# Optimization experiments

Measured on AMD Instinct MI355X. Metric: run time of the kernel, lower is better.

The kernel has to match this reference:

```python
import jax, jax.numpy as jnp
import numpy as np

B, T, H = 4, 2048, 1024
BUD = 512
S = max(8, BUD)
S += S % 2
HALF = S // 2
LOC = max(H, 2 * BUD)


def setup_inputs() -> dict:
    key = jax.random.key(0)
    ks = jax.random.split(key, 16)
    def w(k, i, o):
        return jax.random.normal(k, (i, o), jnp.float32) / np.sqrt(i).astype(np.float32)
    return {
        "x": jax.random.normal(ks[0], (B, T, H), jnp.float32),
        "W_rf": w(ks[1], H, S), "W_ri": w(ks[2], H, S), "W_rv": w(ks[3], H, S),
        "W_rq": w(ks[4], H, S), "W_ro": w(ks[5], S, H),
        "W_sw": w(ks[6], H, S), "W_sg": w(ks[7], H, S), "W_som": w(ks[8], H, HALF),
        "W_sd": w(ks[9], H, S), "W_sq": w(ks[10], H, S), "W_so": w(ks[11], S, H),
        "W_up": w(ks[12], H, LOC), "W_gate": w(ks[13], H, LOC), "W_down": w(ks[14], LOC, H),
        "W_mix": w(ks[15], H, 3),
        "read_init": jnp.zeros((S,), jnp.float32),
        "stable_init": jnp.zeros((S,), jnp.float32),
    }


def reference(x, W_rf, W_ri, W_rv, W_rq, W_ro, W_sw, W_sg, W_som, W_sd, W_sq, W_so,
              W_up, W_gate, W_down, W_mix, read_init, stable_init):
    silu = jax.nn.silu
    # Precompute all per-token projections as batched GEMMs: [B,T,*]
    rf = jnp.tanh(x @ W_rf)                      # read forget
    rg = jax.nn.sigmoid(x @ W_ri)                # read input gate
    rc = silu(x @ W_rv)                          # read candidate
    omega = jnp.pi * jnp.tanh(x @ W_som)         # [B,T,HALF]
    cosw, sinw = jnp.cos(omega), jnp.sin(omega)
    damp = jnp.exp(-jax.nn.softplus(x @ W_sd))
    sg = jax.nn.sigmoid(x @ W_sg)
    sc = silu(x @ W_sw)

    def step(carry, inputs):
        rs, ss = carry
        rf_t, rg_t, rc_t, cw, sw_, dp, sg_t, sc_t = inputs
        rs = rf_t * rs + rg_t * rc_t
        even, odd = ss[:, :HALF], ss[:, HALF:]
        rot = jnp.concatenate([cw * even - sw_ * odd, sw_ * even + cw * odd], axis=-1)
        ss = dp * rot + sg_t * sc_t
        return (rs, ss), (rs, ss)

    init = (jnp.broadcast_to(read_init, (B, S)), jnp.broadcast_to(stable_init, (B, S)))
    seq = tuple(jnp.swapaxes(a, 0, 1) for a in (rf, rg, rc, cosw, sinw, damp, sg, sc))
    _, (rs_seq, ss_seq) = jax.lax.scan(step, init, seq)
    rs_seq = jnp.swapaxes(rs_seq, 0, 1)  # [B,T,S]
    ss_seq = jnp.swapaxes(ss_seq, 0, 1)

    read_f = silu((x @ W_rq) * rs_seq) @ W_ro
    stable_f = silu((x @ W_sq) * ss_seq) @ W_so
    local_f = ((x @ W_up) * silu(x @ W_gate)) @ W_down
    mw = jax.nn.softmax(x @ W_mix, axis=-1)  # [B,T,3]
    out = mw[..., 0:1] * read_f + mw[..., 1:2] * stable_f + mw[..., 2:3] * local_f
    return out
```

## Files before the change

kernel.cpp:

```cpp
#include <hip/hip_runtime.h>

#define B_    4
#define T_    2048
#define H_    1024
#define S_    512
#define HALF_ 256
#define LOC_  1024
#define BT_   8192
#define N1_   6400
#define K1_   1024
#define N2_   1024
#define K2_   2048
#define NCH_  32
#define LC_   64

typedef __attribute__((ext_vector_type(8))) short  bf16x8;
typedef __attribute__((ext_vector_type(4))) float  f32x4;
typedef __attribute__((ext_vector_type(4))) unsigned short u16x4;

__device__ __forceinline__ float b2f(unsigned short u) {
    union { unsigned i; float f; } v; v.i = ((unsigned)u) << 16; return v.f;
}
__device__ __forceinline__ unsigned short f2b(float f) {
    union { float f; unsigned i; } v; v.f = f;
    unsigned r = v.i + 0x7fffu + ((v.i >> 16) & 1u);
    return (unsigned short)(r >> 16);
}
__device__ __forceinline__ float rcp_(float x) { return __builtin_amdgcn_rcpf(x); }
__device__ __forceinline__ float sigm_(float v) { return rcp_(1.f + __expf(-v)); }
__device__ __forceinline__ float silu_(float v) { return v * rcp_(1.f + __expf(-v)); }
__device__ __forceinline__ float tanh_(float v) { return 1.f - 2.f * rcp_(1.f + __expf(2.f * v)); }

__device__ __forceinline__ void gload16(const void* g, void* l) {
    __builtin_amdgcn_global_load_lds(
        (const __attribute__((address_space(1))) void*)g,
        (__attribute__((address_space(3))) void*)l,
        16, 0, 0);
}

__global__ void prep_x(const float* __restrict__ x, const float* __restrict__ Wm,
                       unsigned short* __restrict__ xb, float4* __restrict__ mw) {
    const int row  = blockIdx.x * 4 + (threadIdx.x >> 6);
    const int lane = threadIdx.x & 63;
    const float4* xr = (const float4*)(x + (size_t)row * H_);
    u16x4* xbr = (u16x4*)(xb + (size_t)row * H_);
    float s0 = 0.f, s1 = 0.f, s2 = 0.f;
#pragma unroll
    for (int p = 0; p < 4; p++) {
        const int k4 = p * 64 + lane;
        float4 v = xr[k4];
        u16x4 u;
        u.x = f2b(v.x); u.y = f2b(v.y); u.z = f2b(v.z); u.w = f2b(v.w);
        xbr[k4] = u;
        const int k3 = k4 * 12;
        s0 += v.x * Wm[k3 + 0] + v.y * Wm[k3 + 3] + v.z * Wm[k3 + 6] + v.w * Wm[k3 + 9];
        s1 += v.x * Wm[k3 + 1] + v.y * Wm[k3 + 4] + v.z * Wm[k3 + 7] + v.w * Wm[k3 + 10];
        s2 += v.x * Wm[k3 + 2] + v.y * Wm[k3 + 5] + v.z * Wm[k3 + 8] + v.w * Wm[k3 + 11];
    }
#pragma unroll
    for (int off = 32; off; off >>= 1) {
        s0 += __shfl_down(s0, off);
        s1 += __shfl_down(s1, off);
        s2 += __shfl_down(s2, off);
    }
    if (lane == 0) {
        float m = fmaxf(s0, fmaxf(s1, s2));
        float e0 = __expf(s0 - m), e1 = __expf(s1 - m), e2 = __expf(s2 - m);
        float inv = 1.f / (e0 + e1 + e2);
        mw[row] = (float4){ e0 * inv, e1 * inv, e2 * inv, 0.f };
    }
}

struct TOp { const float* src; int Kw; int Nw; int n_ofs; int k_ofs; int which; };
struct TOps { TOp v[14]; };

__global__ void pack_w_kernel(TOps ops, unsigned short* __restrict__ w1, unsigned short* __restrict__ w2) {
    TOp op = ops.v[blockIdx.z];
    int kt = blockIdx.x * 32, nt = blockIdx.y * 32;
    if (kt >= op.Kw || nt >= op.Nw) return;
    __shared__ float tile[32][33];
    int tx = threadIdx.x & 31, ty = threadIdx.x >> 5;
#pragma unroll
    for (int r = 0; r < 4; r++) {
        int k = kt + ty + r * 8;
        tile[ty + r * 8][tx] = op.src[(size_t)k * op.Nw + nt + tx];
    }
    __syncthreads();
    unsigned short* dst = op.which ? w2 : w1;
    int stride = op.which ? K2_ : K1_;
#pragma unroll
    for (int r = 0; r < 4; r++) {
        int n = nt + ty + r * 8;
        dst[(size_t)(op.n_ofs + n) * stride + op.k_ofs + kt + tx] = f2b(tile[tx][ty + r * 8]);
    }
}

#define STAGE(kt_, dA, dB) {          \
    gload16(aP0 + (kt_), (dA));       \
    gload16(aP1 + (kt_), (dA) + 512); \
    gload16(bP0 + (kt_), (dB));       \
    gload16(bP1 + (kt_), (dB) + 512); }

#define COMPUTE(sAr, sBr) {                                                            \
    bf16x8 af[4], bfv[4];                                                              \
    _Pragma("unroll")                                                                  \
    for (int m_ = 0; m_ < 4; m_++)                                                     \
        af[m_] = *(const bf16x8*)((sAr) + (wm + m_ * 16 + fr) * 32 + rsl);             \
    _Pragma("unroll")                                                                  \
    for (int n_ = 0; n_ < 4; n_++)                                                     \
        bfv[n_] = *(const bf16x8*)((sBr) + (wn + n_ * 16 + fr) * 32 + rsl);            \
    _Pragma("unroll")                                                                  \
    for (int m_ = 0; m_ < 4; m_++)                                                     \
        _Pragma("unroll")                                                              \
        for (int n_ = 0; n_ < 4; n_++)                                                 \
            acc[m_][n_] = __builtin_amdgcn_mfma_f32_16x16x32_bf16(af[m_], bfv[n_], acc[m_][n_], 0, 0, 0); }

template<int MODE>
__global__ __launch_bounds__(256, 3) void gemm_bf16(
    const unsigned short* __restrict__ A,
    const unsigned short* __restrict__ Bt,
    void* __restrict__ Cout,
    unsigned short* __restrict__ swb,
    const int M, const int N, const int K)
{
    __shared__ __align__(16) char smem[32768];
    unsigned short* sA0 = (unsigned short*)smem;
    unsigned short* sB0 = (unsigned short*)(smem + 8192);
    unsigned short* sA1 = (unsigned short*)(smem + 16384);
    unsigned short* sB1 = (unsigned short*)(smem + 24576);
    const int tid  = threadIdx.x;
    const int wid  = tid >> 6;
    const int lane = tid & 63;

    const int flat = blockIdx.y * gridDim.x + blockIdx.x;
    const int xcd  = flat & 7;
    const int ii   = flat >> 3;
    const int bm   = ((xcd << 3) + (ii & 7)) * 128;
    const int bn   = (ii >> 3) * 128;

    const int wm = (wid >> 1) * 64;
    const int wn = (wid & 1) * 64;

    f32x4 acc[4][4];
#pragma unroll
    for (int m = 0; m < 4; m++)
#pragma unroll
        for (int n = 0; n < 4; n++) acc[m][n] = (f32x4){0.f, 0.f, 0.f, 0.f};

    const int r0 = wid * 32 + (lane >> 2);
    const int sl = ((lane & 3) ^ ((r0 >> 1) & 3)) * 8;
    const unsigned short* aP0 = A  + (size_t)(bm + r0)      * K + sl;
    const unsigned short* aP1 = A  + (size_t)(bm + r0 + 16) * K + sl;
    const unsigned short* bP0 = Bt + (size_t)(bn + r0)      * K + sl;
    const unsigned short* bP1 = Bt + (size_t)(bn + r0 + 16) * K + sl;
    unsigned short* wA0 = sA0 + wid * 1024;
    unsigned short* wB0 = sB0 + wid * 1024;
    unsigned short* wA1 = sA1 + wid * 1024;
    unsigned short* wB1 = sB1 + wid * 1024;

    const int fr  = lane & 15;
    const int h   = lane >> 4;
    const int rsl = (h ^ ((fr >> 1) & 3)) * 8;
    const int nt  = K >> 5;

    STAGE(0, wA0, wB0);
    __syncthreads();
    for (int t = 0; t < nt; t += 2) {
        STAGE((t + 1) * 32, wA1, wB1);
        COMPUTE(sA0, sB0);
        __syncthreads();
        if (t + 2 < nt) STAGE((t + 2) * 32, wA0, wB0);
        COMPUTE(sA1, sB1);
        __syncthreads();
    }

    if (MODE == 0) {
        float* outp = (float*)Cout;
        float* wp = (float*)(smem + wid * 4608);
#pragma unroll
        for (int m = 0; m < 4; m++) {
#pragma unroll
            for (int n = 0; n < 4; n++)
#pragma unroll
                for (int r = 0; r < 4; r++)
                    wp[(h * 4 + r) * 68 + n * 16 + fr] = acc[m][n][r];
#pragma unroll
            for (int rnd = 0; rnd < 4; rnd++) {
                int lr = rnd * 4 + (lane >> 4);
                int lc = (lane & 15) * 4;
                float4 v = *(float4*)&wp[lr * 68 + lc];
                int grow = bm + wm + m * 16 + lr;
                int gcol = bn + wn + lc;
                *(float4*)&outp[(size_t)grow * N + gcol] = v;
            }
        }
    } else {
        int reg;
        if      (bn < 512)  reg = 0;
        else if (bn < 1024) reg = 1;
        else if (bn < 1536) reg = 2;
        else if (bn < 2048) reg = 3;
        else if (bn < 2560) reg = 2;
        else if (bn < 3072) reg = 1;
        else if (bn < 3584) reg = 4;
        else if (bn < 4096) reg = 3;
        else if (bn < 4352) reg = 5;
        else if (bn < 5376) reg = 3;
        else                reg = 2;

        unsigned short* proj = (unsigned short*)Cout;
        unsigned short* wp = (unsigned short*)(smem + wid * 2304);
        const int nsub = (reg == 5) ? 2 : 1;
#pragma unroll
        for (int m = 0; m < 4; m++) {
            for (int sub = 0; sub < nsub; sub++) {
#pragma unroll
                for (int n = 0; n < 4; n++)
#pragma unroll
                    for (int r = 0; r < 4; r++) {
                        float v = acc[m][n][r];
                        float o;
                        if      (reg == 0) o = tanh_(v);
                        else if (reg == 1) o = sigm_(v);
                        else if (reg == 2) o = silu_(v);
                        else if (reg == 3) o = v;
                        else if (reg == 4) o = sigm_(-v);
                        else {
                            float om = 3.14159265358979f * tanh_(v);
                            o = sub ? __sinf(om) : __cosf(om);
                        }
                        wp[(h * 4 + r) * 72 + n * 16 + fr] = f2b(o);
                    }
#pragma unroll
                for (int p = 0; p < 2; p++) {
                    int lr = p * 8 + (lane >> 3);
                    int lc = (lane & 7) * 8;
                    bf16x8 v = *(bf16x8*)(wp + lr * 72 + lc);
                    int grow = bm + wm + m * 16 + lr;
                    int gcol = bn + wn + lc;
                    if (sub == 0)
                        *(bf16x8*)(proj + (size_t)grow * N + gcol) = v;
                    else
                        *(bf16x8*)(swb + (size_t)grow * HALF_ + (gcol - 4096)) = v;
                }
            }
        }
    }
}

__global__ void scan_pass1(const unsigned short* __restrict__ proj, const unsigned short* __restrict__ swb,
                           float* __restrict__ rsP, float* __restrict__ rsY,
                           float4* __restrict__ ssM, float2* __restrict__ ssY) {
    const int c = blockIdx.x, b = blockIdx.y, z = blockIdx.z, tid = threadIdx.x;
    const int row0 = b * T_ + c * LC_;
    const unsigned short* base = proj + (size_t)row0 * N1_;
    if (z < 2) {
        const int s = z * 256 + tid;
        float P = 1.f, y = 0.f;
#pragma unroll 4
        for (int t = 0; t < LC_; t++) {
            const unsigned short* r = base + (size_t)t * N1_;
            float rf = b2f(r[s]);
            float rg = b2f(r[512 + s]);
            float rc = b2f(r[1024 + s]);
            y = rf * y + rg * rc;
            P *= rf;
        }
        int idx = (b * NCH_ + c) * S_ + s;
        rsP[idx] = P; rsY[idx] = y;
    } else {
        const int p = tid;
        const unsigned short* swr = swb + (size_t)row0 * HALF_;
        float m00 = 1.f, m01 = 0.f, m10 = 0.f, m11 = 1.f, y0 = 0.f, y1 = 0.f;
#pragma unroll 2
        for (int t = 0; t < LC_; t++) {
            const unsigned short* r = base + (size_t)t * N1_;
            float cw  = b2f(r[4096 + p]);
            float sw  = b2f(swr[(size_t)t * HALF_ + p]);
            float de  = b2f(r[3072 + p]);
            float dob = b2f(r[3328 + p]);
            float ge  = b2f(r[2560 + p]);
            float go  = b2f(r[2816 + p]);
            float ce  = b2f(r[2048 + p]);
            float co  = b2f(r[2304 + p]);
            float a = de * cw, bb = -de * sw, cc = dob * sw, dd = dob * cw;
            float ny0 = a * y0 + bb * y1 + ge * ce;
            float ny1 = cc * y0 + dd * y1 + go * co;
            y0 = ny0; y1 = ny1;
            float n00 = a * m00 + bb * m10, n01 = a * m01 + bb * m11;
            float n10 = cc * m00 + dd * m10, n11 = cc * m01 + dd * m11;
            m00 = n00; m01 = n01; m10 = n10; m11 = n11;
        }
        int idx = (b * NCH_ + c) * HALF_ + p;
        ssM[idx] = (float4){m00, m01, m10, m11};
        ssY[idx] = (float2){y0, y1};
    }
}

__global__ void scan_pass2(const float* __restrict__ rsP, const float* __restrict__ rsY,
                           const float4* __restrict__ ssM, const float2* __restrict__ ssY,
                           const float* __restrict__ read_init, const float* __restrict__ stable_init,
                           float* __restrict__ rsStart, float2* __restrict__ ssStart) {
    int id = blockIdx.x * 256 + threadIdx.x;
    if (id < B_ * S_) {
        int b = id / S_, s = id % S_;
        float st = read_init[s];
        for (int c = 0; c < NCH_; c++) {
            int idx = (b * NCH_ + c) * S_ + s;
            rsStart[idx] = st;
            st = rsP[idx] * st + rsY[idx];
        }
    } else {
        id -= B_ * S_;
        int b = id / HALF_, p = id % HALF_;
        float y0 = stable_init[p], y1 = stable_init[p + HALF_];
        for (int c = 0; c < NCH_; c++) {
            int idx = (b * NCH_ + c) * HALF_ + p;
            ssStart[idx] = (float2){y0, y1};
            float4 m = ssM[idx]; float2 u = ssY[idx];
            float ny0 = m.x * y0 + m.y * y1 + u.x;
            float ny1 = m.z * y0 + m.w * y1 + u.y;
            y0 = ny0; y1 = ny1;
        }
    }
}

__global__ void scan_pass3(const unsigned short* __restrict__ proj, const unsigned short* __restrict__ swb,
                           const float* __restrict__ rsStart, const float2* __restrict__ ssStart,
                           const float4* __restrict__ mw, unsigned short* __restrict__ G) {
    const int c = blockIdx.x, b = blockIdx.y, z = blockIdx.z, tid = threadIdx.x;
    const int row0 = b * T_ + c * LC_;
    const unsigned short* base = proj + (size_t)row0 * N1_;
    if (z < 2) {
        const int s = z * 256 + tid;
        float rs = rsStart[(b * NCH_ + c) * S_ + s];
#pragma unroll 4
        for (int t = 0; t < LC_; t++) {
            const size_t row = row0 + t;
            const unsigned short* r = base + (size_t)t * N1_;
            float rf = b2f(r[s]);
            float rg = b2f(r[512 + s]);
            float rc = b2f(r[1024 + s]);
            rs = rf * rs + rg * rc;
            float q  = b2f(r[1536 + s]);
            float zz = q * rs;
            G[row * 2048 + s] = f2b(mw[row].x * silu_(zz));
        }
    } else {
        const int p = tid;
        const unsigned short* swr = swb + (size_t)row0 * HALF_;
        float2 st = ssStart[(b * NCH_ + c) * HALF_ + p];
        float y0 = st.x, y1 = st.y;
#pragma unroll 2
        for (int t = 0; t < LC_; t++) {
            const size_t row = row0 + t;
            const unsigned short* r = base + (size_t)t * N1_;
            float cw  = b2f(r[4096 + p]);
            float sw  = b2f(swr[(size_t)t * HALF_ + p]);
            float de  = b2f(r[3072 + p]);
            float dob = b2f(r[3328 + p]);
            float ge  = b2f(r[2560 + p]);
            float go  = b2f(r[2816 + p]);
            float ce  = b2f(r[2048 + p]);
            float co  = b2f(r[2304 + p]);
            float a = de * cw, bb = -de * sw, cc = dob * sw, dd = dob * cw;
            float ny0 = a * y0 + bb * y1 + ge * ce;
            float ny1 = cc * y0 + dd * y1 + go * co;
            y0 = ny0; y1 = ny1;
            float qe = b2f(r[3584 + p]);
            float qo = b2f(r[3840 + p]);
            float w1v = mw[row].y;
            G[row * 2048 + 512 + p] = f2b(w1v * silu_(qe * y0));
            G[row * 2048 + 768 + p] = f2b(w1v * silu_(qo * y1));
        }
    }
}

__global__ void local_ew(const unsigned short* __restrict__ proj, const float4* __restrict__ mw,
                         unsigned short* __restrict__ G) {
    int i   = blockIdx.x * 256 + threadIdx.x;
    int row = i >> 7;
    int j   = (i & 127) * 8;
    bf16x8 up = *(const bf16x8*)(proj + (size_t)row * N1_ + 4352 + j);
    bf16x8 gs = *(const bf16x8*)(proj + (size_t)row * N1_ + 5376 + j);
    float m2 = mw[row].z;
    bf16x8 o;
#pragma unroll
    for (int e = 0; e < 8; e++)
        o[e] = (short)f2b(m2 * b2f((unsigned short)up[e]) * b2f((unsigned short)gs[e]));
    *(bf16x8*)(G + (size_t)row * 2048 + 1024 + j) = o;
}

extern "C" void kernel_launch(void* const* d_in, const int* in_sizes, int n_in,
                              void* d_out, int out_size, void* d_ws, size_t ws_size,
                              hipStream_t stream) {
    const float* x       = (const float*)d_in[0];
    const float* W_rf    = (const float*)d_in[1];
    const float* W_ri    = (const float*)d_in[2];
    const float* W_rv    = (const float*)d_in[3];
    const float* W_rq    = (const float*)d_in[4];
    const float* W_ro    = (const float*)d_in[5];
    const float* W_sw    = (const float*)d_in[6];
    const float* W_sg    = (const float*)d_in[7];
    const float* W_som   = (const float*)d_in[8];
    const float* W_sd    = (const float*)d_in[9];
    const float* W_sq    = (const float*)d_in[10];
    const float* W_so    = (const float*)d_in[11];
    const float* W_up    = (const float*)d_in[12];
    const float* W_gate  = (const float*)d_in[13];
    const float* W_down  = (const float*)d_in[14];
    const float* W_mix   = (const float*)d_in[15];
    const float* read_init   = (const float*)d_in[16];
    const float* stable_init = (const float*)d_in[17];

    char* ws = (char*)d_ws;
    size_t off = 0;
    auto alloc = [&](size_t bytes) -> void* {
        void* p = ws + off;
        off = (off + bytes + 255) & ~(size_t)255;
        return p;
    };
    unsigned short* xb   = (unsigned short*)alloc((size_t)BT_ * H_ * 2);
    unsigned short* w1   = (unsigned short*)alloc((size_t)N1_ * K1_ * 2);
    unsigned short* w2   = (unsigned short*)alloc((size_t)N2_ * K2_ * 2);
    unsigned short* proj = (unsigned short*)alloc((size_t)BT_ * N1_ * 2);
    unsigned short* swb  = (unsigned short*)alloc((size_t)BT_ * HALF_ * 2);
    float4*         mw   = (float4*)alloc((size_t)BT_ * 16);
    unsigned short* G    = (unsigned short*)alloc((size_t)BT_ * 2048 * 2);
    float*  rsP     = (float*) alloc((size_t)B_ * NCH_ * S_ * 4);
    float*  rsY     = (float*) alloc((size_t)B_ * NCH_ * S_ * 4);
    float4* ssM     = (float4*)alloc((size_t)B_ * NCH_ * HALF_ * 16);
    float2* ssY     = (float2*)alloc((size_t)B_ * NCH_ * HALF_ * 8);
    float*  rsStart = (float*) alloc((size_t)B_ * NCH_ * S_ * 4);
    float2* ssStart = (float2*)alloc((size_t)B_ * NCH_ * HALF_ * 8);
    if (off > ws_size) return;

    prep_x<<<BT_ / 4, 256, 0, stream>>>(x, W_mix, xb, mw);

    TOps ops;
    int i = 0;
    auto add = [&](const float* s, int Kw, int Nw, int n_ofs, int k_ofs, int which) {
        ops.v[i].src = s; ops.v[i].Kw = Kw; ops.v[i].Nw = Nw;
        ops.v[i].n_ofs = n_ofs; ops.v[i].k_ofs = k_ofs; ops.v[i].which = which; i++;
    };
    add(W_rf,  1024,  512,    0,    0, 0);
    add(W_ri,  1024,  512,  512,    0, 0);
    add(W_rv,  1024,  512, 1024,    0, 0);
    add(W_rq,  1024,  512, 1536,    0, 0);
    add(W_sw,  1024,  512, 2048,    0, 0);
    add(W_sg,  1024,  512, 2560,    0, 0);
    add(W_sd,  1024,  512, 3072,    0, 0);
    add(W_sq,  1024,  512, 3584,    0, 0);
    add(W_som, 1024,  256, 4096,    0, 0);
    add(W_up,  1024, 1024, 4352,    0, 0);
    add(W_gate,1024, 1024, 5376,    0, 0);
    add(W_ro,   512, 1024,    0,    0, 1);
    add(W_so,   512, 1024,    0,  512, 1);
    add(W_down,1024, 1024,    0, 1024, 1);
    pack_w_kernel<<<dim3(32, 32, 14), 256, 0, stream>>>(ops, w1, w2);

    gemm_bf16<1><<<dim3(N1_ / 128, BT_ / 128), 256, 0, stream>>>(xb, w1, (void*)proj, swb, BT_, N1_, K1_);

    scan_pass1<<<dim3(NCH_, B_, 3), 256, 0, stream>>>(proj, swb, rsP, rsY, ssM, ssY);
    scan_pass2<<<12, 256, 0, stream>>>(rsP, rsY, ssM, ssY, read_init, stable_init, rsStart, ssStart);
    scan_pass3<<<dim3(NCH_, B_, 3), 256, 0, stream>>>(proj, swb, rsStart, ssStart, mw, G);

    local_ew<<<(BT_ * LOC_ / 8) / 256, 256, 0, stream>>>(proj, mw, G);

    gemm_bf16<0><<<dim3(N2_ / 128, BT_ / 128), 256, 0, stream>>>(G, w2, d_out, nullptr, BT_, N2_, K2_);
}
```

Baseline: 273.7 us.

## Fuse local gated-MLP elementwise into projection GEMM epilogue via interleaved up/gate weights

Packs the W_up and W_gate columns interleaved in 16-column groups so each warp's accumulator holds matching up and gate values. The first GEMM's epilogue then computes mix-weight * up * silu(gate) directly and writes bf16 into G, and the separate local_ew kernel is removed. This avoids writing up/gate projections to proj and reading them back in another kernel. In exchange the epilogue gains per-row mw loads and a new store pattern.

```diff
diff --git a/kernel.cpp b/kernel.cpp
--- a/kernel.cpp
+++ b/kernel.cpp
@@ -71,7 +71,7 @@
     }
 }
 
-struct TOp { const float* src; int Kw; int Nw; int n_ofs; int k_ofs; int which; };
+struct TOp { const float* src; int Kw; int Nw; int n_ofs; int k_ofs; int which; int ilv; };
 struct TOps { TOp v[14]; };
 
 __global__ void pack_w_kernel(TOps ops, unsigned short* __restrict__ w1, unsigned short* __restrict__ w2) {
@@ -91,7 +91,12 @@
 #pragma unroll
     for (int r = 0; r < 4; r++) {
         int n = nt + ty + r * 8;
-        dst[(size_t)(op.n_ofs + n) * stride + op.k_ofs + kt + tx] = f2b(tile[tx][ty + r * 8]);
+        int dcol;
+        if (op.ilv)
+            dcol = op.n_ofs + ((n >> 4) << 5) + ((op.ilv == 2) ? 16 : 0) + (n & 15);
+        else
+            dcol = op.n_ofs + n;
+        dst[(size_t)dcol * stride + op.k_ofs + kt + tx] = f2b(tile[tx][ty + r * 8]);
     }
 }
 
@@ -121,6 +126,8 @@
     const unsigned short* __restrict__ Bt,
     void* __restrict__ Cout,
     unsigned short* __restrict__ swb,
+    const float4* __restrict__ mwp,
+    unsigned short* __restrict__ G,
     const int M, const int N, const int K)
 {
     __shared__ __align__(16) char smem[32768];
@@ -205,43 +212,67 @@
         else if (bn < 3584) reg = 4;
         else if (bn < 4096) reg = 3;
         else if (bn < 4352) reg = 5;
-        else if (bn < 5376) reg = 3;
-        else                reg = 2;
+        else                reg = 6;
 
         unsigned short* proj = (unsigned short*)Cout;
-        unsigned short* wp = (unsigned short*)(smem + wid * 2304);
-        const int nsub = (reg == 5) ? 2 : 1;
-#pragma unroll
-        for (int m = 0; m < 4; m++) {
-            for (int sub = 0; sub < nsub; sub++) {
-#pragma unroll
-                for (int n = 0; n < 4; n++)
+        if (reg == 6) {
+            unsigned short* wp = (unsigned short*)(smem + wid * 2304);
+            const int sb = (bn + wn - 4352) >> 5;
+#pragma unroll
+            for (int m = 0; m < 4; m++) {
+#pragma unroll
+                for (int pr = 0; pr < 2; pr++)
 #pragma unroll
                     for (int r = 0; r < 4; r++) {
-                        float v = acc[m][n][r];
-                        float o;
-                        if      (reg == 0) o = tanh_(v);
-                        else if (reg == 1) o = sigm_(v);
-                        else if (reg == 2) o = silu_(v);
-                        else if (reg == 3) o = v;
-                        else if (reg == 4) o = sigm_(-v);
-                        else {
-                            float om = 3.14159265358979f * tanh_(v);
-                            o = sub ? __sinf(om) : __cosf(om);
+                        int row = bm + wm + m * 16 + h * 4 + r;
+                        float m2 = mwp[row].z;
+                        float up = acc[m][pr * 2][r];
+                        float gt = acc[m][pr * 2 + 1][r];
+                        wp[(h * 4 + r) * 40 + pr * 16 + fr] = f2b(m2 * up * silu_(gt));
+                    }
+                {
+                    int lr = lane >> 2;
+                    int lc = (lane & 3) * 8;
+                    bf16x8 v = *(bf16x8*)(wp + lr * 40 + lc);
+                    int grow = bm + wm + m * 16 + lr;
+                    *(bf16x8*)(G + (size_t)grow * 2048 + 1024 + sb * 16 + lc) = v;
+                }
+            }
+        } else {
+            unsigned short* wp = (unsigned short*)(smem + wid * 2304);
+            const int nsub = (reg == 5) ? 2 : 1;
+#pragma unroll
+            for (int m = 0; m < 4; m++) {
+                for (int sub = 0; sub < nsub; sub++) {
+#pragma unroll
+                    for (int n = 0; n < 4; n++)
+#pragma unroll
+                        for (int r = 0; r < 4; r++) {
+                            float v = acc[m][n][r];
+                            float o;
+                            if      (reg == 0) o = tanh_(v);
+                            else if (reg == 1) o = sigm_(v);
+                            else if (reg == 2) o = silu_(v);
+                            else if (reg == 3) o = v;
+                            else if (reg == 4) o = sigm_(-v);
+                            else {
+                                float om = 3.14159265358979f * tanh_(v);
+                                o = sub ? __sinf(om) : __cosf(om);
+                            }
+                            wp[(h * 4 + r) * 72 + n * 16 + fr] = f2b(o);
                         }
-                        wp[(h * 4 + r) * 72 + n * 16 + fr] = f2b(o);
+#pragma unroll
+                    for (int p = 0; p < 2; p++) {
+                        int lr = p * 8 + (lane >> 3);
+                        int lc = (lane & 7) * 8;
+                        bf16x8 v = *(bf16x8*)(wp + lr * 72 + lc);
+                        int grow = bm + wm + m * 16 + lr;
+                        int gcol = bn + wn + lc;
+                        if (sub == 0)
+                            *(bf16x8*)(proj + (size_t)grow * N + gcol) = v;
+                        else
+                            *(bf16x8*)(swb + (size_t)grow * HALF_ + (gcol - 4096)) = v;
                     }
-#pragma unroll
-                for (int p = 0; p < 2; p++) {
-                    int lr = p * 8 + (lane >> 3);
-                    int lc = (lane & 7) * 8;
-                    bf16x8 v = *(bf16x8*)(wp + lr * 72 + lc);
-                    int grow = bm + wm + m * 16 + lr;
-                    int gcol = bn + wn + lc;
-                    if (sub == 0)
-                        *(bf16x8*)(proj + (size_t)grow * N + gcol) = v;
-                    else
-                        *(bf16x8*)(swb + (size_t)grow * HALF_ + (gcol - 4096)) = v;
                 }
             }
         }
@@ -376,21 +407,6 @@
     }
 }
 
-__global__ void local_ew(const unsigned short* __restrict__ proj, const float4* __restrict__ mw,
-                         unsigned short* __restrict__ G) {
-    int i   = blockIdx.x * 256 + threadIdx.x;
-    int row = i >> 7;
-    int j   = (i & 127) * 8;
-    bf16x8 up = *(const bf16x8*)(proj + (size_t)row * N1_ + 4352 + j);
-    bf16x8 gs = *(const bf16x8*)(proj + (size_t)row * N1_ + 5376 + j);
-    float m2 = mw[row].z;
-    bf16x8 o;
-#pragma unroll
-    for (int e = 0; e < 8; e++)
-        o[e] = (short)f2b(m2 * b2f((unsigned short)up[e]) * b2f((unsigned short)gs[e]));
-    *(bf16x8*)(G + (size_t)row * 2048 + 1024 + j) = o;
-}
-
 extern "C" void kernel_launch(void* const* d_in, const int* in_sizes, int n_in,
                               void* d_out, int out_size, void* d_ws, size_t ws_size,
                               hipStream_t stream) {
@@ -439,33 +455,34 @@
 
     TOps ops;
     int i = 0;
-    auto add = [&](const float* s, int Kw, int Nw, int n_ofs, int k_ofs, int which) {
+    auto add = [&](const float* s, int Kw, int Nw, int n_ofs, int k_ofs, int which, int ilv) {
         ops.v[i].src = s; ops.v[i].Kw = Kw; ops.v[i].Nw = Nw;
-        ops.v[i].n_ofs = n_ofs; ops.v[i].k_ofs = k_ofs; ops.v[i].which = which; i++;
+        ops.v[i].n_ofs = n_ofs; ops.v[i].k_ofs = k_ofs; ops.v[i].which = which;
+        ops.v[i].ilv = ilv; i++;
     };
-    add(W_rf,  1024,  512,    0,    0, 0);
-    add(W_ri,  1024,  512,  512,    0, 0);
-    add(W_rv,  1024,  512, 1024,    0, 0);
-    add(W_rq,  1024,  512, 1536,    0, 0);
-    add(W_sw,  1024,  512, 2048,    0, 0);
-    add(W_sg,  1024,  512, 2560,    0, 0);
-    add(W_sd,  1024,  512, 3072,    0, 0);
-    add(W_sq,  1024,  512, 3584,    0, 0);
-    add(W_som, 1024,  256, 4096,    0, 0);
-    add(W_up,  1024, 1024, 4352,    0, 0);
-    add(W_gate,1024, 1024, 5376,    0, 0);
-    add(W_ro,   512, 1024,    0,    0, 1);
-    add(W_so,   512, 1024,    0,  512, 1);
-    add(W_down,1024, 1024,    0, 1024, 1);
+    add(W_rf,  1024,  512,    0,    0, 0, 0);
+    add(W_ri,  1024,  512,  512,    0, 0, 0);
+    add(W_rv,  1024,  512, 1024,    0, 0, 0);
+    add(W_rq,  1024,  512, 1536,    0, 0, 0);
+    add(W_sw,  1024,  512, 2048,    0, 0, 0);
+    add(W_sg,  1024,  512, 2560,    0, 0, 0);
+    add(W_sd,  1024,  512, 3072,    0, 0, 0);
+    add(W_sq,  1024,  512, 3584,    0, 0, 0);
+    add(W_som, 1024,  256, 4096,    0, 0, 0);
+    add(W_up,  1024, 1024, 4352,    0, 0, 1);
+    add(W_gate,1024, 1024, 4352,    0, 0, 2);
+    add(W_ro,   512, 1024,    0,    0, 1, 0);
+    add(W_so,   512, 1024,    0,  512, 1, 0);
+    add(W_down,1024, 1024,    0, 1024, 1, 0);
     pack_w_kernel<<<dim3(32, 32, 14), 256, 0, stream>>>(ops, w1, w2);
 
-    gemm_bf16<1><<<dim3(N1_ / 128, BT_ / 128), 256, 0, stream>>>(xb, w1, (void*)proj, swb, BT_, N1_, K1_);
+    gemm_bf16<1><<<dim3(N1_ / 128, BT_ / 128), 256, 0, stream>>>(
+        xb, w1, (void*)proj, swb, mw, G, BT_, N1_, K1_);
 
     scan_pass1<<<dim3(NCH_, B_, 3), 256, 0, stream>>>(proj, swb, rsP, rsY, ssM, ssY);
     scan_pass2<<<12, 256, 0, stream>>>(rsP, rsY, ssM, ssY, read_init, stable_init, rsStart, ssStart);
     scan_pass3<<<dim3(NCH_, B_, 3), 256, 0, stream>>>(proj, swb, rsStart, ssStart, mw, G);
 
-    local_ew<<<(BT_ * LOC_ / 8) / 256, 256, 0, stream>>>(proj, mw, G);
-
-    gemm_bf16<0><<<dim3(N2_ / 128, BT_ / 128), 256, 0, stream>>>(G, w2, d_out, nullptr, BT_, N2_, K2_);
-}
+    gemm_bf16<0><<<dim3(N2_ / 128, BT_ / 128), 256, 0, stream>>>(
+        G, w2, d_out, nullptr, nullptr, nullptr, BT_, N2_, K2_);
+}
```

After: 230.5 us. -15.8%, faster.
